# Kernel tuning notes

Measured on AMD Instinct MI355X. Metric: run time of the kernel, lower is better.

The kernel has to match this reference:

```python
import jax, jax.numpy as jnp
import numpy as np
from jax import lax


def setup_inputs() -> dict:
    key = jax.random.key(0)
    k1, k2, k3, k4, k5 = jax.random.split(key, 5)
    B, T, V, E, U = 64, 256, 32000, 256, 1024
    x = jax.random.randint(k1, (B, T), 0, V)          # token ids; 0 = pad (mask_zero=True)
    hidden = jnp.zeros((B, U), dtype=jnp.float32)      # initialize_hidden_state()
    emb = jax.random.normal(k2, (V, E), dtype=jnp.float32) * 0.05
    W = jax.random.normal(k3, (E, 3 * U), dtype=jnp.float32) * 0.05   # input kernel [z|r|h]
    Uk = jax.random.normal(k4, (U, 3 * U), dtype=jnp.float32) * 0.05  # recurrent kernel
    b = jax.random.normal(k5, (2, 3 * U), dtype=jnp.float32) * 0.05   # [input_bias, recurrent_bias] (reset_after=True)
    return {"x": x, "hidden": hidden, "emb": emb, "W": W, "U": Uk, "b": b}


def reference(x, hidden, emb, W, U, b):
    # Embedding with mask_zero=True: mask out pad tokens in the GRU scan.
    mask = (x != 0)                              # [B, T] bool
    xe = emb[x]                                  # [B, T, E]
    # Precompute all input projections in one big GEMM.
    xproj = jnp.einsum("bte,eu->btu", xe, W) + b[0]   # [B, T, 3U]
    nU = U.shape[0]

    def step(h, inp):
        xp, m = inp                              # xp: [B, 3U], m: [B]
        rec = h @ U + b[1]                       # [B, 3U]
        xz, xr, xh = jnp.split(xp, 3, axis=-1)
        rz, rr, rh = jnp.split(rec, 3, axis=-1)
        z = jax.nn.sigmoid(xz + rz)
        r = jax.nn.sigmoid(xr + rr)
        hh = jnp.tanh(xh + r * rh)               # reset_after=True form
        h_new = z * h + (1.0 - z) * hh
        h_new = jnp.where(m[:, None], h_new, h)  # masked steps carry state/output through
        return h_new, h_new

    state, outs = lax.scan(step, hidden,
                           (jnp.swapaxes(xproj, 0, 1), jnp.swapaxes(mask, 0, 1)))
    output = jnp.swapaxes(outs, 0, 1)            # [B, T, U]
    return output, state
```

## Files before the change

### kernel.cpp

```cpp
#include <hip/hip_runtime.h>
#include <hip/hip_cooperative_groups.h>

#define BB 64
#define TT 256
#define EE 256
#define NU 1024
#define N3 3072

typedef __attribute__((ext_vector_type(8))) short bf16x8;
typedef __attribute__((ext_vector_type(4))) float f32x4;

__device__ __forceinline__ unsigned short f2bf(float f) {
    unsigned u = __float_as_uint(f);
    return (unsigned short)((u + 0x7FFFu + ((u >> 16) & 1u)) >> 16);
}

__global__ __launch_bounds__(256) void upack_kernel(
    const float* __restrict__ U, float* __restrict__ up)
{
    __shared__ float t32[32][33];
    const int c0 = blockIdx.x * 32, k0 = blockIdx.y * 32;
    const int tx = threadIdx.x & 31, ty = threadIdx.x >> 5;
    #pragma unroll
    for (int i = 0; i < 4; ++i) {
        int k = ty + i * 8;
        t32[k][tx] = U[(size_t)(k0 + k) * N3 + c0 + tx];
    }
    __syncthreads();
    #pragma unroll
    for (int i = 0; i < 4; ++i) {
        int cl = ty + i * 8;
        int c = c0 + cl;
        int u = c & 1023, g = c >> 10;
        up[(size_t)(u * 3 + g) * NU + k0 + tx] = t32[tx][cl];
    }
}

__global__ __launch_bounds__(64) void tokT_kernel(
    const int* __restrict__ x, int* __restrict__ xT)
{
    const int t = blockIdx.x, b = threadIdx.x;
    xT[t * BB + b] = x[b * TT + t];
}

__global__ __launch_bounds__(256) void hinit_kernel(
    const float* __restrict__ hidden, unsigned short* __restrict__ hb0,
    unsigned* __restrict__ cnt)
{
    const int u = blockIdx.x * 4 + (threadIdx.x >> 6);
    const int b = threadIdx.x & 63;
    hb0[((u >> 3) * 64 + b) * 8 + (u & 7)] = f2bf(hidden[(size_t)b * NU + u]);
    if (blockIdx.x == 0) {
        cnt[threadIdx.x] = 0u;
        cnt[threadIdx.x + 256] = 0u;
    }
}

__global__ __launch_bounds__(256) void xprojT_kernel(
    const int* __restrict__ x, const float* __restrict__ emb,
    const float* __restrict__ W, const float* __restrict__ bias,
    float* __restrict__ xpT)
{
    __shared__ float AsT[32][132];
    __shared__ float Ws[32][132];
    __shared__ int toks[128];

    const int tid = threadIdx.x;
    const int mt = blockIdx.x / 24, nt = blockIdx.x % 24;
    const int m0 = mt * 128, n0 = nt * 128;

    if (tid < 128) {
        int mg = m0 + tid;
        toks[tid] = x[(mg & 63) * TT + (mg >> 6)];
    }
    __syncthreads();

    const int tx = tid & 15, ty = tid >> 4;
    float acc[8][8] = {};

    for (int kb = 0; kb < 8; ++kb) {
        const int k0 = kb * 32;
        if (kb) __syncthreads();
        #pragma unroll
        for (int i = 0; i < 4; ++i) {
            int idx = tid + 256 * i;
            int m = idx >> 3, c4 = idx & 7;
            float4 av = *(const float4*)(emb + (size_t)toks[m] * EE + k0 + c4 * 4);
            AsT[c4 * 4 + 0][m] = av.x; AsT[c4 * 4 + 1][m] = av.y;
            AsT[c4 * 4 + 2][m] = av.z; AsT[c4 * 4 + 3][m] = av.w;
            int r = idx >> 5, w4 = idx & 31;
            *(float4*)&Ws[r][w4 * 4] =
                *(const float4*)(W + (size_t)(k0 + r) * N3 + n0 + w4 * 4);
        }
        __syncthreads();
        #pragma unroll 8
        for (int kk = 0; kk < 32; ++kk) {
            float a8[8], w8[8];
            *(float4*)a8       = *(const float4*)&AsT[kk][ty * 8];
            *(float4*)(a8 + 4) = *(const float4*)&AsT[kk][ty * 8 + 4];
            *(float4*)w8       = *(const float4*)&Ws[kk][tx * 8];
            *(float4*)(w8 + 4) = *(const float4*)&Ws[kk][tx * 8 + 4];
            #pragma unroll
            for (int i = 0; i < 8; ++i)
                #pragma unroll
                for (int j = 0; j < 8; ++j) acc[i][j] += a8[i] * w8[j];
        }
    }

    float b8[8];
    *(float4*)b8       = *(const float4*)(bias + n0 + tx * 8);
    *(float4*)(b8 + 4) = *(const float4*)(bias + n0 + tx * 8 + 4);
    const int t0 = mt * 2 + (ty >> 3);
    const int bb0 = (ty & 7) * 8;
    #pragma unroll
    for (int j = 0; j < 8; ++j) {
        const int c = n0 + tx * 8 + j;
        float4 lo, hi;
        lo.x = acc[0][j] + b8[j]; lo.y = acc[1][j] + b8[j];
        lo.z = acc[2][j] + b8[j]; lo.w = acc[3][j] + b8[j];
        hi.x = acc[4][j] + b8[j]; hi.y = acc[5][j] + b8[j];
        hi.z = acc[6][j] + b8[j]; hi.w = acc[7][j] + b8[j];
        size_t base = ((size_t)t0 * N3 + c) * BB + bb0;
        *(float4*)(xpT + base)     = lo;
        *(float4*)(xpT + base + 4) = hi;
    }
}

__global__ __launch_bounds__(512) void gru_persist(
    const int* __restrict__ xT, const float* __restrict__ upack,
    const float* __restrict__ bias, float* xpT,
    float* __restrict__ out, const float* __restrict__ hidden,
    unsigned short* hb0, unsigned short* hb1, unsigned* cnt)
{
    __shared__ float red[8 * 1024];
    __shared__ unsigned short hstage[256];

    const int tid = threadIdx.x;
    const int u0 = blockIdx.x * 4;
    const int w = tid >> 6;
    const int lane = tid & 63;

    bf16x8 af[4];
    {
        const int row = lane & 15;
        #pragma unroll
        for (int s = 0; s < 4; ++s) {
            if (row < 12) {
                const int R = (u0 + (row & 3)) * 3 + (row >> 2);
                const int k0 = w * 128 + s * 32 + (lane >> 4) * 8;
                const float* p = upack + (size_t)R * NU + k0;
                float4 v0 = *(const float4*)p;
                float4 v1 = *(const float4*)(p + 4);
                af[s] = (bf16x8){ (short)f2bf(v0.x), (short)f2bf(v0.y),
                                  (short)f2bf(v0.z), (short)f2bf(v0.w),
                                  (short)f2bf(v1.x), (short)f2bf(v1.y),
                                  (short)f2bf(v1.z), (short)f2bf(v1.w) };
            } else {
                af[s] = (bf16x8){0, 0, 0, 0, 0, 0, 0, 0};
            }
        }
    }

    float hold = 0.f, brz = 0.f, brr = 0.f, brh = 0.f;
    float xz = 0.f, xr = 0.f, xh = 0.f; int tok = 1;
    if (tid < 256) {
        hold = hidden[(size_t)lane * NU + u0 + w];
        brz = bias[N3 + 0 * NU + u0 + w];
        brr = bias[N3 + 1 * NU + u0 + w];
        brh = bias[N3 + 2 * NU + u0 + w];
        size_t xb = ((size_t)0 * N3 + u0 + w) * BB + lane;
        xz = xpT[xb];
        xr = xpT[xb + (size_t)NU * BB];
        xh = xpT[xb + (size_t)2 * NU * BB];
        tok = xT[0 * BB + lane];
    }
    float* state_out = out + (size_t)BB * TT * NU;
    __syncthreads();

    const unsigned short* hc = hb0;
    unsigned short* hn = hb1;

    for (int t = 0; t < TT; ++t) {
        bf16x8 bv[4][4];
        #pragma unroll
        for (int n = 0; n < 4; ++n)
            #pragma unroll
            for (int s = 0; s < 4; ++s) {
                const int ew = w * 16 + s * 4 + (lane >> 4);
                bv[n][s] = *(const bf16x8*)(hc +
                    (size_t)(ew * 64 + n * 16 + (lane & 15)) * 8);
            }

        f32x4 c0 = {0.f, 0.f, 0.f, 0.f}, c1 = c0, c2 = c0, c3 = c0;
        #pragma unroll
        for (int s = 0; s < 4; ++s) {
            c0 = __builtin_amdgcn_mfma_f32_16x16x32_bf16(af[s], bv[0][s], c0, 0, 0, 0);
            c1 = __builtin_amdgcn_mfma_f32_16x16x32_bf16(af[s], bv[1][s], c1, 0, 0, 0);
            c2 = __builtin_amdgcn_mfma_f32_16x16x32_bf16(af[s], bv[2][s], c2, 0, 0, 0);
            c3 = __builtin_amdgcn_mfma_f32_16x16x32_bf16(af[s], bv[3][s], c3, 0, 0, 0);
        }
        #pragma unroll
        for (int r = 0; r < 4; ++r) {
            red[w * 1024 + (0 * 4 + r) * 64 + lane] = c0[r];
            red[w * 1024 + (1 * 4 + r) * 64 + lane] = c1[r];
            red[w * 1024 + (2 * 4 + r) * 64 + lane] = c2[r];
            red[w * 1024 + (3 * 4 + r) * 64 + lane] = c3[r];
        }
        __syncthreads();

        if (tid < 256) {
            const int du = w, b = lane;
            float rz = brz, rr = brr, rh = brh;
            const int base = ((b >> 4) * 4 + du) * 64 + (b & 15);
            #pragma unroll
            for (int q = 0; q < 8; ++q) {
                rz += red[q * 1024 + base];
                rr += red[q * 1024 + base + 16];
                rh += red[q * 1024 + base + 32];
            }
            float z  = 1.f / (1.f + expf(-(xz + rz)));
            float r  = 1.f / (1.f + expf(-(xr + rr)));
            float hh = tanhf(xh + r * rh);
            float hnew = z * hold + (1.f - z) * hh;
            if (tok == 0) hnew = hold;

            __hip_atomic_store(&xpT[((size_t)t * N3 + u0 + du) * BB + b], hnew,
                               __ATOMIC_RELAXED, __HIP_MEMORY_SCOPE_SYSTEM);
            if (t == TT - 1)
                __hip_atomic_store(&state_out[(size_t)b * NU + u0 + du], hnew,
                                   __ATOMIC_RELAXED, __HIP_MEMORY_SCOPE_SYSTEM);
            hstage[b * 4 + du] = f2bf(hnew);
            hold = hnew;
        }
        __syncthreads();

        if (w == 4) {
            uint2 hv = *(const uint2*)&hstage[lane * 4];
            unsigned long long hv64 =
                ((unsigned long long)hv.y << 32) | (unsigned long long)hv.x;
            __hip_atomic_store(
                (unsigned long long*)(hn + (size_t)(u0 >> 3) * 512 + (u0 & 7) + lane * 8),
                hv64, __ATOMIC_RELAXED, __HIP_MEMORY_SCOPE_SYSTEM);
        }

        __builtin_amdgcn_s_waitcnt(0);
        __syncthreads();

        if (tid < 256 && t + 1 < TT) {
            size_t xb = ((size_t)(t + 1) * N3 + u0 + w) * BB + lane;
            xz = xpT[xb];
            xr = xpT[xb + (size_t)NU * BB];
            xh = xpT[xb + (size_t)2 * NU * BB];
            tok = xT[(t + 1) * BB + lane];
        }

        if (tid == 0) {
            const unsigned g = (unsigned)blockIdx.x >> 5;
            unsigned old = __hip_atomic_fetch_add(&cnt[g * 32], 1u,
                               __ATOMIC_RELAXED, __HIP_MEMORY_SCOPE_SYSTEM);
            if (old == 32u * (unsigned)t + 31u)
                __hip_atomic_fetch_add(&cnt[256], 1u,
                               __ATOMIC_RELAXED, __HIP_MEMORY_SCOPE_SYSTEM);
            const unsigned tgt = 8u * ((unsigned)t + 1u);
            unsigned v;
            long guard = 0;
            do {
                v = __hip_atomic_load(&cnt[256],
                                      __ATOMIC_RELAXED, __HIP_MEMORY_SCOPE_SYSTEM);
                if (v < tgt) __builtin_amdgcn_s_sleep(1);
            } while (v < tgt && ++guard < (1L << 24));
            __builtin_amdgcn_fence(__ATOMIC_ACQUIRE, "");
        }
        __syncthreads();

        const unsigned short* tmp = hc; hc = hn; hn = (unsigned short*)tmp;
    }
}

__global__ __launch_bounds__(256) void outT_kernel(
    const float* __restrict__ xpT, float* __restrict__ out)
{
    __shared__ float tile[64][65];
    const int t = blockIdx.x, u0 = blockIdx.y * 64;
    const int lane = threadIdx.x & 63, row = threadIdx.x >> 6;
    #pragma unroll
    for (int r = row; r < 64; r += 4)
        tile[r][lane] = xpT[((size_t)t * N3 + u0 + r) * BB + lane];
    __syncthreads();
    #pragma unroll
    for (int b = row; b < 64; b += 4)
        out[((size_t)b * TT + t) * NU + u0 + lane] = tile[lane][b];
}

extern "C" void kernel_launch(void* const* d_in, const int* in_sizes, int n_in,
                              void* d_out, int out_size, void* d_ws, size_t ws_size,
                              hipStream_t stream) {
    const int*   x      = (const int*)d_in[0];
    const float* hidden = (const float*)d_in[1];
    const float* emb    = (const float*)d_in[2];
    const float* W      = (const float*)d_in[3];
    const float* U      = (const float*)d_in[4];
    const float* bvec   = (const float*)d_in[5];

    float* out = (float*)d_out;

    float*          xpT   = (float*)d_ws;
    float*          upck  = xpT + (size_t)16384 * N3;
    unsigned short* hb0   = (unsigned short*)(upck + (size_t)3 * NU * NU);
    unsigned short* hb1   = hb0 + (size_t)NU * BB;
    int*            xT    = (int*)(hb1 + (size_t)NU * BB);
    unsigned*       cnt   = (unsigned*)(xT + TT * BB);

    upack_kernel<<<dim3(96, 32), dim3(256), 0, stream>>>(U, upck);
    tokT_kernel<<<dim3(TT), dim3(64), 0, stream>>>(x, xT);
    hinit_kernel<<<dim3(256), dim3(256), 0, stream>>>(hidden, hb0, cnt);
    xprojT_kernel<<<dim3(3072), dim3(256), 0, stream>>>(x, emb, W, bvec, xpT);

    void* args[] = {(void*)&xT, (void*)&upck, (void*)&bvec, (void*)&xpT,
                    (void*)&out, (void*)&hidden, (void*)&hb0, (void*)&hb1,
                    (void*)&cnt};
    hipLaunchCooperativeKernel((const void*)gru_persist, dim3(256), dim3(512),
                               args, 0, stream);

    outT_kernel<<<dim3(TT, 16), dim3(256), 0, stream>>>(xpT, out);
}
```

Measured before the change: 2.293 ms.

## Use 64 persistent GRU blocks of 16 units each with a flat barrier

```diff
diff --git a/kernel.cpp b/kernel.cpp
--- a/kernel.cpp
+++ b/kernel.cpp
@@ -132,47 +132,47 @@
     float* __restrict__ out, const float* __restrict__ hidden,
     unsigned short* hb0, unsigned short* hb1, unsigned* cnt)
 {
-    __shared__ float red[8 * 1024];
-    __shared__ unsigned short hstage[256];
+    __shared__ f32x4 red2[6144];
+    __shared__ unsigned short hstage[64 * 20];
 
     const int tid = threadIdx.x;
-    const int u0 = blockIdx.x * 4;
+    const int U0 = blockIdx.x * 16;
     const int w = tid >> 6;
     const int lane = tid & 63;
 
-    bf16x8 af[4];
+    const int gdu = tid >> 5;
+    const int gbA = tid & 31;
+
+    bf16x8 af[3][4];
     {
-        const int row = lane & 15;
-        #pragma unroll
-        for (int s = 0; s < 4; ++s) {
-            if (row < 12) {
-                const int R = (u0 + (row & 3)) * 3 + (row >> 2);
+        const int du = lane & 15;
+        #pragma unroll
+        for (int g = 0; g < 3; ++g)
+            #pragma unroll
+            for (int s = 0; s < 4; ++s) {
                 const int k0 = w * 128 + s * 32 + (lane >> 4) * 8;
-                const float* p = upack + (size_t)R * NU + k0;
+                const float* p = upack + (size_t)((U0 + du) * 3 + g) * NU + k0;
                 float4 v0 = *(const float4*)p;
                 float4 v1 = *(const float4*)(p + 4);
-                af[s] = (bf16x8){ (short)f2bf(v0.x), (short)f2bf(v0.y),
-                                  (short)f2bf(v0.z), (short)f2bf(v0.w),
-                                  (short)f2bf(v1.x), (short)f2bf(v1.y),
-                                  (short)f2bf(v1.z), (short)f2bf(v1.w) };
-            } else {
-                af[s] = (bf16x8){0, 0, 0, 0, 0, 0, 0, 0};
+                af[g][s] = (bf16x8){ (short)f2bf(v0.x), (short)f2bf(v0.y),
+                                     (short)f2bf(v0.z), (short)f2bf(v0.w),
+                                     (short)f2bf(v1.x), (short)f2bf(v1.y),
+                                     (short)f2bf(v1.z), (short)f2bf(v1.w) };
             }
-        }
-    }
-
-    float hold = 0.f, brz = 0.f, brr = 0.f, brh = 0.f;
-    float xz = 0.f, xr = 0.f, xh = 0.f; int tok = 1;
-    if (tid < 256) {
-        hold = hidden[(size_t)lane * NU + u0 + w];
-        brz = bias[N3 + 0 * NU + u0 + w];
-        brr = bias[N3 + 1 * NU + u0 + w];
-        brh = bias[N3 + 2 * NU + u0 + w];
-        size_t xb = ((size_t)0 * N3 + u0 + w) * BB + lane;
-        xz = xpT[xb];
-        xr = xpT[xb + (size_t)NU * BB];
-        xh = xpT[xb + (size_t)2 * NU * BB];
-        tok = xT[0 * BB + lane];
+    }
+
+    float holdA = hidden[(size_t)gbA * NU + U0 + gdu];
+    float holdB = hidden[(size_t)(gbA + 32) * NU + U0 + gdu];
+    const float brz = bias[N3 + 0 * NU + U0 + gdu];
+    const float brr = bias[N3 + 1 * NU + U0 + gdu];
+    const float brh = bias[N3 + 2 * NU + U0 + gdu];
+    float xzA, xrA, xhA, xzB, xrB, xhB; int tokA, tokB;
+    {
+        size_t xb = ((size_t)0 * N3 + U0 + gdu) * BB + gbA;
+        xzA = xpT[xb];                      xzB = xpT[xb + 32];
+        xrA = xpT[xb + (size_t)NU * BB];    xrB = xpT[xb + (size_t)NU * BB + 32];
+        xhA = xpT[xb + (size_t)2 * NU * BB];xhB = xpT[xb + (size_t)2 * NU * BB + 32];
+        tokA = xT[0 * BB + gbA];            tokB = xT[0 * BB + gbA + 32];
     }
     float* state_out = out + (size_t)BB * TT * NU;
     __syncthreads();
@@ -191,84 +191,116 @@
                     (size_t)(ew * 64 + n * 16 + (lane & 15)) * 8);
             }
 
-        f32x4 c0 = {0.f, 0.f, 0.f, 0.f}, c1 = c0, c2 = c0, c3 = c0;
-        #pragma unroll
-        for (int s = 0; s < 4; ++s) {
-            c0 = __builtin_amdgcn_mfma_f32_16x16x32_bf16(af[s], bv[0][s], c0, 0, 0, 0);
-            c1 = __builtin_amdgcn_mfma_f32_16x16x32_bf16(af[s], bv[1][s], c1, 0, 0, 0);
-            c2 = __builtin_amdgcn_mfma_f32_16x16x32_bf16(af[s], bv[2][s], c2, 0, 0, 0);
-            c3 = __builtin_amdgcn_mfma_f32_16x16x32_bf16(af[s], bv[3][s], c3, 0, 0, 0);
-        }
-        #pragma unroll
-        for (int r = 0; r < 4; ++r) {
-            red[w * 1024 + (0 * 4 + r) * 64 + lane] = c0[r];
-            red[w * 1024 + (1 * 4 + r) * 64 + lane] = c1[r];
-            red[w * 1024 + (2 * 4 + r) * 64 + lane] = c2[r];
-            red[w * 1024 + (3 * 4 + r) * 64 + lane] = c3[r];
-        }
-        __syncthreads();
-
-        if (tid < 256) {
-            const int du = w, b = lane;
-            float rz = brz, rr = brr, rh = brh;
-            const int base = ((b >> 4) * 4 + du) * 64 + (b & 15);
+        f32x4 c[3][4];
+        #pragma unroll
+        for (int g = 0; g < 3; ++g)
+            #pragma unroll
+            for (int n = 0; n < 4; ++n) c[g][n] = (f32x4){0.f, 0.f, 0.f, 0.f};
+        #pragma unroll
+        for (int s = 0; s < 4; ++s)
+            #pragma unroll
+            for (int g = 0; g < 3; ++g)
+                #pragma unroll
+                for (int n = 0; n < 4; ++n)
+                    c[g][n] = __builtin_amdgcn_mfma_f32_16x16x32_bf16(
+                        af[g][s], bv[n][s], c[g][n], 0, 0, 0);
+
+        #pragma unroll
+        for (int g = 0; g < 3; ++g)
+            #pragma unroll
+            for (int n = 0; n < 4; ++n)
+                red2[((w * 3 + g) * 4 + n) * 64 + lane] = c[g][n];
+        __syncthreads();
+
+        {
+            const int lA = (gdu >> 2) * 16 + (gbA & 15);
+            const int rsub = gdu & 3;
+            const int nA = gbA >> 4;
+            float rzA = brz, rrA = brr, rhA = brh;
+            float rzB = brz, rrB = brr, rhB = brh;
             #pragma unroll
             for (int q = 0; q < 8; ++q) {
-                rz += red[q * 1024 + base];
-                rr += red[q * 1024 + base + 16];
-                rh += red[q * 1024 + base + 32];
+                const int qb = (q * 3) * 4;
+                float vA, vB;
+                vA = ((const float*)&red2[(qb + 0 * 4 + nA) * 64 + lA])[rsub];
+                vB = ((const float*)&red2[(qb + 0 * 4 + nA + 2) * 64 + lA])[rsub];
+                rzA += vA; rzB += vB;
+                vA = ((const float*)&red2[(qb + 1 * 4 + nA) * 64 + lA])[rsub];
+                vB = ((const float*)&red2[(qb + 1 * 4 + nA + 2) * 64 + lA])[rsub];
+                rrA += vA; rrB += vB;
+                vA = ((const float*)&red2[(qb + 2 * 4 + nA) * 64 + lA])[rsub];
+                vB = ((const float*)&red2[(qb + 2 * 4 + nA + 2) * 64 + lA])[rsub];
+                rhA += vA; rhB += vB;
             }
-            float z  = 1.f / (1.f + expf(-(xz + rz)));
-            float r  = 1.f / (1.f + expf(-(xr + rr)));
-            float hh = tanhf(xh + r * rh);
-            float hnew = z * hold + (1.f - z) * hh;
-            if (tok == 0) hnew = hold;
-
-            __hip_atomic_store(&xpT[((size_t)t * N3 + u0 + du) * BB + b], hnew,
+            float zA  = 1.f / (1.f + expf(-(xzA + rzA)));
+            float rA  = 1.f / (1.f + expf(-(xrA + rrA)));
+            float hhA = tanhf(xhA + rA * rhA);
+            float hnewA = zA * holdA + (1.f - zA) * hhA;
+            if (tokA == 0) hnewA = holdA;
+            float zB  = 1.f / (1.f + expf(-(xzB + rzB)));
+            float rB  = 1.f / (1.f + expf(-(xrB + rrB)));
+            float hhB = tanhf(xhB + rB * rhB);
+            float hnewB = zB * holdB + (1.f - zB) * hhB;
+            if (tokB == 0) hnewB = holdB;
+
+            size_t ob = ((size_t)t * N3 + U0 + gdu) * BB + gbA;
+            __hip_atomic_store(&xpT[ob], hnewA,
                                __ATOMIC_RELAXED, __HIP_MEMORY_SCOPE_SYSTEM);
-            if (t == TT - 1)
-                __hip_atomic_store(&state_out[(size_t)b * NU + u0 + du], hnew,
+            __hip_atomic_store(&xpT[ob + 32], hnewB,
+                               __ATOMIC_RELAXED, __HIP_MEMORY_SCOPE_SYSTEM);
+            if (t == TT - 1) {
+                __hip_atomic_store(&state_out[(size_t)gbA * NU + U0 + gdu], hnewA,
                                    __ATOMIC_RELAXED, __HIP_MEMORY_SCOPE_SYSTEM);
-            hstage[b * 4 + du] = f2bf(hnew);
-            hold = hnew;
-        }
-        __syncthreads();
-
-        if (w == 4) {
-            uint2 hv = *(const uint2*)&hstage[lane * 4];
-            unsigned long long hv64 =
-                ((unsigned long long)hv.y << 32) | (unsigned long long)hv.x;
-            __hip_atomic_store(
-                (unsigned long long*)(hn + (size_t)(u0 >> 3) * 512 + (u0 & 7) + lane * 8),
-                hv64, __ATOMIC_RELAXED, __HIP_MEMORY_SCOPE_SYSTEM);
+                __hip_atomic_store(&state_out[(size_t)(gbA + 32) * NU + U0 + gdu], hnewB,
+                                   __ATOMIC_RELAXED, __HIP_MEMORY_SCOPE_SYSTEM);
+            }
+            hstage[gbA * 20 + gdu] = f2bf(hnewA);
+            hstage[(gbA + 32) * 20 + gdu] = f2bf(hnewB);
+            holdA = hnewA; holdB = hnewB;
+        }
+        __syncthreads();
+
+        if (w == 4 || w == 5) {
+            const int g2 = w - 4;
+            unsigned long long lo =
+                *(const unsigned long long*)&hstage[lane * 20 + 8 * g2];
+            unsigned long long hi =
+                *(const unsigned long long*)&hstage[lane * 20 + 8 * g2 + 4];
+            unsigned short* dst = hn + ((size_t)((U0 >> 3) + g2) * 64 + lane) * 8;
+            __hip_atomic_store((unsigned long long*)dst, lo,
+                               __ATOMIC_RELAXED, __HIP_MEMORY_SCOPE_SYSTEM);
+            __hip_atomic_store((unsigned long long*)(dst + 4), hi,
+                               __ATOMIC_RELAXED, __HIP_MEMORY_SCOPE_SYSTEM);
         }
 
         __builtin_amdgcn_s_waitcnt(0);
         __syncthreads();
 
-        if (tid < 256 && t + 1 < TT) {
-            size_t xb = ((size_t)(t + 1) * N3 + u0 + w) * BB + lane;
-            xz = xpT[xb];
-            xr = xpT[xb + (size_t)NU * BB];
-            xh = xpT[xb + (size_t)2 * NU * BB];
-            tok = xT[(t + 1) * BB + lane];
+        if (t + 1 < TT) {
+            size_t xb = ((size_t)(t + 1) * N3 + U0 + gdu) * BB + gbA;
+            xzA = xpT[xb];                      xzB = xpT[xb + 32];
+            xrA = xpT[xb + (size_t)NU * BB];    xrB = xpT[xb + (size_t)NU * BB + 32];
+            xhA = xpT[xb + (size_t)2 * NU * BB];xhB = xpT[xb + (size_t)2 * NU * BB + 32];
+            tokA = xT[(t + 1) * BB + gbA];      tokB = xT[(t + 1) * BB + gbA + 32];
         }
 
         if (tid == 0) {
-            const unsigned g = (unsigned)blockIdx.x >> 5;
-            unsigned old = __hip_atomic_fetch_add(&cnt[g * 32], 1u,
-                               __ATOMIC_RELAXED, __HIP_MEMORY_SCOPE_SYSTEM);
-            if (old == 32u * (unsigned)t + 31u)
-                __hip_atomic_fetch_add(&cnt[256], 1u,
-                               __ATOMIC_RELAXED, __HIP_MEMORY_SCOPE_SYSTEM);
+            const unsigned g = (unsigned)blockIdx.x >> 3;
+            __hip_atomic_fetch_add(&cnt[g * 32], 1u,
+                                   __ATOMIC_RELAXED, __HIP_MEMORY_SCOPE_SYSTEM);
             const unsigned tgt = 8u * ((unsigned)t + 1u);
-            unsigned v;
+            unsigned mn;
             long guard = 0;
             do {
-                v = __hip_atomic_load(&cnt[256],
-                                      __ATOMIC_RELAXED, __HIP_MEMORY_SCOPE_SYSTEM);
-                if (v < tgt) __builtin_amdgcn_s_sleep(1);
-            } while (v < tgt && ++guard < (1L << 24));
+                mn = 0xffffffffu;
+                #pragma unroll
+                for (int g8 = 0; g8 < 8; ++g8) {
+                    unsigned v = __hip_atomic_load(&cnt[g8 * 32],
+                                  __ATOMIC_RELAXED, __HIP_MEMORY_SCOPE_SYSTEM);
+                    mn = v < mn ? v : mn;
+                }
+                if (mn < tgt) __builtin_amdgcn_s_sleep(1);
+            } while (mn < tgt && ++guard < (1L << 24));
             __builtin_amdgcn_fence(__ATOMIC_ACQUIRE, "");
         }
         __syncthreads();
@@ -319,7 +351,7 @@
     void* args[] = {(void*)&xT, (void*)&upck, (void*)&bvec, (void*)&xpT,
                     (void*)&out, (void*)&hidden, (void*)&hb0, (void*)&hb1,
                     (void*)&cnt};
-    hipLaunchCooperativeKernel((const void*)gru_persist, dim3(256), dim3(512),
+    hipLaunchCooperativeKernel((const void*)gru_persist, dim3(64), dim3(512),
                                args, 0, stream);
 
     outT_kernel<<<dim3(TT, 16), dim3(256), 0, stream>>>(xpT, out);
```

New measurement: 2.051 ms. 1.12x faster.
